# Optimization experiments

Measured on AMD Instinct MI355X. Metric: run time of the kernel, lower is better.

The kernel has to match this reference:

```python
import jax, jax.numpy as jnp
import numpy as np

TOPK = 2


def setup_inputs() -> dict:
    key = jax.random.key(0)
    k1, k2, k3, k4, k5 = jax.random.split(key, 5)
    D, H, E = 1024, 1408, 8
    hidden_states = jax.random.normal(k1, (2, 1024, D), dtype=jnp.float32)
    gate_w = jax.random.normal(k2, (E, D), dtype=jnp.float32) * 0.02
    w1g = jax.random.normal(k3, (E, D, H), dtype=jnp.float32) * 0.02
    w1u = jax.random.normal(k4, (E, D, H), dtype=jnp.float32) * 0.02
    w2 = jax.random.normal(k5, (E, H, D), dtype=jnp.float32) * 0.02
    return {"hidden_states": hidden_states, "gate_w": gate_w, "w1g": w1g, "w1u": w1u, "w2": w2}


def reference(hidden_states, gate_w, w1g, w1u, w2):
    # hidden_states: [B, S, D]; expert weights: w1g/w1u [E, D, H], w2 [E, H, D]
    B, S, D = hidden_states.shape
    E = gate_w.shape[0]
    x = hidden_states.reshape(-1, D)  # [T, D]
    T = x.shape[0]

    # --- MoEGate: softmax scores, top-k routing (no topk renorm) ---
    logits = x @ gate_w.T                      # [T, E]
    scores = jax.nn.softmax(logits, axis=-1)   # [T, E]
    topk_w, topk_idx = jax.lax.top_k(scores, TOPK)  # [T, K]

    # Per-token combine coefficient for each expert: coeff[t, e] = sum_k w[t,k] * (idx[t,k]==e)
    coeff = jnp.zeros((T, E), dtype=x.dtype).at[jnp.arange(T)[:, None], topk_idx].add(topk_w)

    # --- Grouped expert MLP (swiglu): identical math to permute + grouped GEMM + unpermute ---
    g = jnp.einsum('td,edh->teh', x, w1g)      # [T, E, H]
    u = jnp.einsum('td,edh->teh', x, w1u)      # [T, E, H]
    h = jax.nn.silu(g) * u                     # [T, E, H]
    y = jnp.einsum('teh,te,ehd->td', h, coeff, w2)  # [T, D]
    return y.reshape(B, S, D)
```

## Files before the change

kernel.cpp:

```cpp
#include <hip/hip_runtime.h>

#define TOK 2048
#define DDIM 1024
#define HDIM 1408
#define ENUM 8
#define NSLOT (2 * TOK)
#define UP_NB 22
#define UP_KS 32
#define DN_NB 16
#define DN_KS 44
#define DN_KH 22
#define TC_W1_BLK 2816
#define TC_ALL_BLK 4224
#define GATE_BLK 512

typedef unsigned int uint;
typedef unsigned short ushort;
typedef unsigned long long ull;

using bf16x8 = __attribute__((ext_vector_type(8))) __bf16;
using f32x4  = __attribute__((ext_vector_type(4))) float;

__device__ __forceinline__ float silu_f(float g) {
    return g / (1.0f + __expf(-g));
}

__device__ __forceinline__ ushort cvt_bf16(float f) {
    uint u = __float_as_uint(f);
    u += 0x7FFFu + ((u >> 16) & 1u);
    return (ushort)(u >> 16);
}

__device__ __forceinline__ void gl2lds16(const void* g, void* l) {
    __builtin_amdgcn_global_load_lds(
        (const __attribute__((address_space(1))) uint*)g,
        (__attribute__((address_space(3))) uint*)l, 16, 0, 0);
}

__global__ __launch_bounds__(256) void tcast_gate_kernel(
    const float* __restrict__ w1g, const float* __restrict__ w1u,
    const float* __restrict__ w2, ushort* __restrict__ BgP,
    ushort* __restrict__ BuP, ushort* __restrict__ W2P,
    const float* __restrict__ x, const float* __restrict__ gw,
    int* __restrict__ tinfo, float* __restrict__ wslot, ushort* __restrict__ xb)
{
    const int bid = blockIdx.x;
    const int tid = threadIdx.x;

    if (bid < TC_ALL_BLK) {
        const float* src; ushort* dst; int N, KS, NB, e, nb, ks0;
        if (bid < TC_W1_BLK) {
            const int z = bid / 176;
            const int rem = bid - z * 176;
            src = (z & 8) ? w1u : w1g;
            dst = (z & 8) ? BuP : BgP;
            N = HDIM; KS = UP_KS; NB = UP_NB; e = z & 7;
            nb = rem >> 3; ks0 = (rem & 7) * 4;
        } else {
            const int b2 = bid - TC_W1_BLK;
            e = b2 / 176;
            const int rem = b2 - e * 176;
            src = w2; dst = W2P;
            N = DDIM; KS = DN_KS; NB = DN_NB;
            nb = rem / 11; ks0 = (rem - nb * 11) * 4;
        }
        const int kg = tid & 3;
        const int nn = tid >> 2;
        const float* sb = src + (size_t)e * ((size_t)KS * 32) * N + nb * 64 + nn;
        ushort* db = dst + ((((size_t)e * NB + nb) * KS) + ks0) * 2048 + nn * 32 + kg * 8;
#pragma unroll
        for (int ksi = 0; ksi < 4; ++ksi) {
            const float* st = sb + (size_t)((ks0 + ksi) * 32 + kg * 8) * N;
            float v[8];
#pragma unroll
            for (int j = 0; j < 8; ++j) v[j] = st[(size_t)j * N];
            ushort o[8];
#pragma unroll
            for (int j = 0; j < 8; ++j) o[j] = cvt_bf16(v[j]);
            *(uint4*)(db + ksi * 2048) = *(uint4*)o;
        }
        return;
    }

    const int t = (bid - TC_ALL_BLK) * 4 + (tid >> 6);
    const int lane = tid & 63;
    const float* xr = x + (size_t)t * DDIM;
    ushort* xbr = xb + (size_t)t * DDIM;
    float xv[16];
#pragma unroll
    for (int i = 0; i < 16; ++i) xv[i] = xr[lane + 64 * i];
#pragma unroll
    for (int i = 0; i < 16; ++i) xbr[lane + 64 * i] = cvt_bf16(xv[i]);
    float logit[ENUM];
#pragma unroll
    for (int e = 0; e < ENUM; ++e) {
        const float* gr = gw + (size_t)e * DDIM;
        float acc = 0.f;
#pragma unroll
        for (int i = 0; i < 16; ++i) acc += xv[i] * gr[lane + 64 * i];
#pragma unroll
        for (int s = 32; s > 0; s >>= 1) acc += __shfl_xor(acc, s, 64);
        logit[e] = acc;
    }
    if (lane == 0) {
        float mx = logit[0];
#pragma unroll
        for (int e = 1; e < ENUM; ++e) mx = fmaxf(mx, logit[e]);
        float p[ENUM]; float se = 0.f;
#pragma unroll
        for (int e = 0; e < ENUM; ++e) { p[e] = __expf(logit[e] - mx); se += p[e]; }
        float inv = 1.0f / se;
#pragma unroll
        for (int e = 0; e < ENUM; ++e) p[e] *= inv;
        int i0 = 0;
#pragma unroll
        for (int e = 1; e < ENUM; ++e) if (p[e] > p[i0]) i0 = e;
        int i1 = (i0 == 0) ? 1 : 0;
#pragma unroll
        for (int e = 0; e < ENUM; ++e) if (e != i0 && p[e] > p[i1]) i1 = e;
        tinfo[t] = i0 | (i1 << 4);
        wslot[(t << 1)] = p[i0];
        wslot[(t << 1) | 1] = p[i1];
    }
}

__global__ __launch_bounds__(256) void gate2_kernel(
    const int* __restrict__ tinfo, int* __restrict__ counts, int* __restrict__ toks)
{
    const int e = blockIdx.x;
    const int tid = threadIdx.x;
    const int lane = tid & 63;
    __shared__ int cnt;
    if (tid == 0) cnt = 0;
    __syncthreads();
    int* te = toks + e * TOK;
    for (int t = tid; t < TOK; t += 256) {
        int info = tinfo[t];
        ull m0 = __ballot((info & 15) == e);
        if (m0) {
            int base;
            if (lane == 0) base = atomicAdd(&cnt, __popcll(m0));
            base = __shfl(base, 0, 64);
            if ((m0 >> lane) & 1)
                te[base + __popcll(m0 & ((1ull << lane) - 1))] = (t << 1);
        }
        ull m1 = __ballot((info >> 4) == e);
        if (m1) {
            int base;
            if (lane == 0) base = atomicAdd(&cnt, __popcll(m1));
            base = __shfl(base, 0, 64);
            if ((m1 >> lane) & 1)
                te[base + __popcll(m1 & ((1ull << lane) - 1))] = (t << 1) | 1;
        }
    }
    __syncthreads();
    if (tid == 0) counts[e] = cnt;
}

__global__ __launch_bounds__(256, 4) void up_mfma(
    const ushort* __restrict__ xb, const ushort* __restrict__ BgP,
    const ushort* __restrict__ BuP, const int* __restrict__ counts,
    const int* __restrict__ toks, ushort* __restrict__ Hbuf)
{
    const int e = blockIdx.z;
    const int cnt = counts[e];
    const int m0 = blockIdx.y * 128;
    if (m0 >= cnt) return;
    const int nb = blockIdx.x;
    const int tid = threadIdx.x;
    const int w = tid >> 6;
    const int lane = tid & 63;
    const int q = lane >> 4;
    const int l15 = lane & 15;
    const int wr = w >> 1;
    const int wc = w & 1;

    __shared__ ushort As[2][128][32];
    __shared__ ushort Bgs[2][64][32];
    __shared__ ushort Bus[2][64][32];
    __shared__ int rowslot[128];

    if (tid < 128) rowslot[tid] = (m0 + tid < cnt) ? toks[e * TOK + m0 + tid] : -1;
    __syncthreads();

    const int srow = w * 16 + (lane >> 2);
    const int clog = (((lane & 3) + 4 - ((srow >> 1) & 3)) & 3) * 8;
    const int as0 = rowslot[srow];
    const int as1 = rowslot[srow + 64];
    const ushort* agp0 = xb + (size_t)(as0 < 0 ? 0 : (as0 >> 1)) * DDIM + clog;
    const ushort* agp1 = xb + (size_t)(as1 < 0 ? 0 : (as1 >> 1)) * DDIM + clog;
    const size_t tb = (size_t)(e * UP_NB + nb) * UP_KS * 2048;
    const ushort* bgp = BgP + tb + srow * 32 + clog;
    const ushort* bup = BuP + tb + srow * 32 + clog;

    const int coff = ((q + (l15 >> 1)) & 3) * 8;

    f32x4 accg[4][2], accu[4][2];
#pragma unroll
    for (int i = 0; i < 4; ++i)
#pragma unroll
        for (int j = 0; j < 2; ++j) { accg[i][j] = (f32x4)0.f; accu[i][j] = (f32x4)0.f; }

#define UP_PREFETCH(KSV, B)                                        \
    {                                                              \
        gl2lds16(agp0 + (KSV) * 32, &As[B][w * 16][0]);            \
        gl2lds16(agp1 + (KSV) * 32, &As[B][64 + w * 16][0]);       \
        gl2lds16(bgp + (size_t)(KSV) * 2048, &Bgs[B][w * 16][0]);  \
        gl2lds16(bup + (size_t)(KSV) * 2048, &Bus[B][w * 16][0]);  \
    }

    UP_PREFETCH(0, 0);
    __syncthreads();

    for (int ks = 0; ks < UP_KS; ++ks) {
        const int cur = ks & 1;
        const int nxt = cur ^ 1;
        if (ks + 1 < UP_KS) UP_PREFETCH(ks + 1, nxt);

        bf16x8 a[4], bg[2], bu[2];
#pragma unroll
        for (int mi = 0; mi < 4; ++mi)
            a[mi] = *(const bf16x8*)&As[cur][wr * 64 + mi * 16 + l15][coff];
#pragma unroll
        for (int ni = 0; ni < 2; ++ni) {
            bg[ni] = *(const bf16x8*)&Bgs[cur][wc * 32 + ni * 16 + l15][coff];
            bu[ni] = *(const bf16x8*)&Bus[cur][wc * 32 + ni * 16 + l15][coff];
        }
#pragma unroll
        for (int mi = 0; mi < 4; ++mi)
#pragma unroll
            for (int ni = 0; ni < 2; ++ni) {
                accg[mi][ni] = __builtin_amdgcn_mfma_f32_16x16x32_bf16(a[mi], bg[ni], accg[mi][ni], 0, 0, 0);
                accu[mi][ni] = __builtin_amdgcn_mfma_f32_16x16x32_bf16(a[mi], bu[ni], accu[mi][ni], 0, 0, 0);
            }
        __syncthreads();
    }
#undef UP_PREFETCH

#pragma unroll
    for (int mi = 0; mi < 4; ++mi) {
#pragma unroll
        for (int r = 0; r < 4; ++r) {
            int ml = wr * 64 + mi * 16 + q * 4 + r;
            int slot = rowslot[ml];
            if (slot < 0) continue;
            ushort* hrow = Hbuf + (size_t)slot * HDIM + nb * 64 + wc * 32 + l15;
#pragma unroll
            for (int ni = 0; ni < 2; ++ni)
                hrow[ni * 16] = cvt_bf16(silu_f(accg[mi][ni][r]) * accu[mi][ni][r]);
        }
    }
}

__global__ __launch_bounds__(256, 4) void down_mfma(
    const ushort* __restrict__ Hbuf, const ushort* __restrict__ W2P,
    const int* __restrict__ counts, const int* __restrict__ toks,
    float* __restrict__ Ybuf)
{
    const int z = blockIdx.z;
    const int e = z >> 1;
    const int kh = z & 1;
    const int cnt = counts[e];
    const int m0 = blockIdx.y * 128;
    if (m0 >= cnt) return;
    const int nb = blockIdx.x;
    const int tid = threadIdx.x;
    const int w = tid >> 6;
    const int lane = tid & 63;
    const int q = lane >> 4;
    const int l15 = lane & 15;
    const int wr = w >> 1;
    const int wc = w & 1;

    __shared__ ushort As[2][128][32];
    __shared__ ushort Bs[2][128][32];
    __shared__ int rowslot[128];

    if (tid < 128) rowslot[tid] = (m0 + tid < cnt) ? toks[e * TOK + m0 + tid] : -1;
    __syncthreads();

    const int srow = w * 16 + (lane >> 2);
    const int clog = (((lane & 3) + 4 - ((srow >> 1) & 3)) & 3) * 8;
    const int as0 = rowslot[srow];
    const int as1 = rowslot[srow + 64];
    const ushort* agp0 = Hbuf + (size_t)(as0 < 0 ? 0 : as0) * HDIM + kh * (DN_KH * 32) + clog;
    const ushort* agp1 = Hbuf + (size_t)(as1 < 0 ? 0 : as1) * HDIM + kh * (DN_KH * 32) + clog;
    const int nb2 = nb * 2;
    const ushort* bp0 = W2P + ((size_t)(e * DN_NB + nb2) * DN_KS + kh * DN_KH) * 2048 + srow * 32 + clog;
    const ushort* bp1 = W2P + ((size_t)(e * DN_NB + nb2 + 1) * DN_KS + kh * DN_KH) * 2048 + srow * 32 + clog;

    const int coff = ((q + (l15 >> 1)) & 3) * 8;

    f32x4 acc[4][4];
#pragma unroll
    for (int i = 0; i < 4; ++i)
#pragma unroll
        for (int j = 0; j < 4; ++j) acc[i][j] = (f32x4)0.f;

#define DN_PREFETCH(KSV, B)                                           \
    {                                                                 \
        gl2lds16(agp0 + (KSV) * 32, &As[B][w * 16][0]);               \
        gl2lds16(agp1 + (KSV) * 32, &As[B][64 + w * 16][0]);          \
        gl2lds16(bp0 + (size_t)(KSV) * 2048, &Bs[B][w * 16][0]);      \
        gl2lds16(bp1 + (size_t)(KSV) * 2048, &Bs[B][64 + w * 16][0]); \
    }

    DN_PREFETCH(0, 0);
    __syncthreads();

    for (int ks = 0; ks < DN_KH; ++ks) {
        const int cur = ks & 1;
        const int nxt = cur ^ 1;
        if (ks + 1 < DN_KH) DN_PREFETCH(ks + 1, nxt);

        bf16x8 a[4], b[4];
#pragma unroll
        for (int mi = 0; mi < 4; ++mi)
            a[mi] = *(const bf16x8*)&As[cur][wr * 64 + mi * 16 + l15][coff];
#pragma unroll
        for (int ni = 0; ni < 4; ++ni)
            b[ni] = *(const bf16x8*)&Bs[cur][wc * 64 + ni * 16 + l15][coff];
#pragma unroll
        for (int mi = 0; mi < 4; ++mi)
#pragma unroll
            for (int ni = 0; ni < 4; ++ni)
                acc[mi][ni] = __builtin_amdgcn_mfma_f32_16x16x32_bf16(a[mi], b[ni], acc[mi][ni], 0, 0, 0);
        __syncthreads();
    }
#undef DN_PREFETCH

    float* Yp = Ybuf + (size_t)kh * NSLOT * DDIM;
#pragma unroll
    for (int mi = 0; mi < 4; ++mi) {
#pragma unroll
        for (int r = 0; r < 4; ++r) {
            int ml = wr * 64 + mi * 16 + q * 4 + r;
            int slot = rowslot[ml];
            if (slot < 0) continue;
            float* yr = Yp + (size_t)slot * DDIM + nb * 128 + wc * 64 + l15;
#pragma unroll
            for (int ni = 0; ni < 4; ++ni)
                yr[ni * 16] = acc[mi][ni][r];
        }
    }
}

__global__ __launch_bounds__(256) void combine_kernel(
    const float* __restrict__ Ybuf, const float* __restrict__ wslot,
    float* __restrict__ y)
{
    const int t = blockIdx.x;
    const int j = threadIdx.x * 4;
    const float w0 = wslot[2 * t];
    const float w1 = wslot[2 * t + 1];
    const float* y00 = Ybuf + ((size_t)2 * t) * DDIM + j;
    const float* y01 = Ybuf + ((size_t)2 * t + 1) * DDIM + j;
    const float* y10 = y00 + (size_t)NSLOT * DDIM;
    const float* y11 = y01 + (size_t)NSLOT * DDIM;
    float4 a0 = *(const float4*)y00;
    float4 b0 = *(const float4*)y01;
    float4 a1 = *(const float4*)y10;
    float4 b1 = *(const float4*)y11;
    float4 o;
    o.x = w0 * (a0.x + a1.x) + w1 * (b0.x + b1.x);
    o.y = w0 * (a0.y + a1.y) + w1 * (b0.y + b1.y);
    o.z = w0 * (a0.z + a1.z) + w1 * (b0.z + b1.z);
    o.w = w0 * (a0.w + a1.w) + w1 * (b0.w + b1.w);
    *(float4*)(y + (size_t)t * DDIM + j) = o;
}

extern "C" void kernel_launch(void* const* d_in, const int* in_sizes, int n_in,
                              void* d_out, int out_size, void* d_ws, size_t ws_size,
                              hipStream_t stream) {
    const float* x   = (const float*)d_in[0];
    const float* gw  = (const float*)d_in[1];
    const float* w1g = (const float*)d_in[2];
    const float* w1u = (const float*)d_in[3];
    const float* w2  = (const float*)d_in[4];
    float* y = (float*)d_out;
    char* ws = (char*)d_ws;

    size_t off = 0;
    int*    counts = (int*)(ws + off);   off += 256;
    int*    toks   = (int*)(ws + off);   off += (size_t)ENUM * TOK * 4;
    float*  wslot  = (float*)(ws + off); off += (size_t)NSLOT * 4;
    int*    tinfo  = (int*)(ws + off);   off += (size_t)TOK * 4;
    off = (off + 255) & ~(size_t)255;
    ushort* xb     = (ushort*)(ws + off); off += (size_t)TOK * DDIM * 2;
    size_t regA = off;
    ushort* BgP  = (ushort*)(ws + regA);
    ushort* BuP  = (ushort*)(ws + regA + (size_t)ENUM * DDIM * HDIM * 2);
    float*  Ybuf = (float*)(ws + regA);
    off = regA + (size_t)2 * ENUM * DDIM * HDIM * 2;
    ushort* W2P  = (ushort*)(ws + off);  off += (size_t)ENUM * HDIM * DDIM * 2;
    ushort* Hbuf = (ushort*)(ws + off);

    tcast_gate_kernel<<<TC_ALL_BLK + GATE_BLK, 256, 0, stream>>>(
        w1g, w1u, w2, BgP, BuP, W2P, x, gw, tinfo, wslot, xb);
    gate2_kernel<<<ENUM, 256, 0, stream>>>(tinfo, counts, toks);

    up_mfma<<<dim3(UP_NB, TOK / 128, ENUM), 256, 0, stream>>>(xb, BgP, BuP, counts, toks, Hbuf);
    down_mfma<<<dim3(DDIM / 128, TOK / 128, 16), 256, 0, stream>>>(Hbuf, W2P, counts, toks, Ybuf);
    combine_kernel<<<TOK, 256, 0, stream>>>(Ybuf, wslot, y);
}
```

Baseline: 256.2 us.

## Fuse routing scatter into gate kernel and combine via atomic adds in down GEMM

The separate gate2 routing kernel is removed. Each gate block now handles 64 tokens, builds a local histogram, reserves per-expert ranges with global atomics, and writes the token lists itself. The combine kernel and the Ybuf intermediate are also removed: down_mfma scales each row by its routing weight and atomically adds it into the zero-initialised output. This cuts two launches and a large fp32 round trip through memory. In exchange it adds two memsets, many float atomics on the output, non-deterministic summation order, and fewer gate blocks (32), each doing more serial work.

```diff
diff --git a/kernel.cpp b/kernel.cpp
--- a/kernel.cpp
+++ b/kernel.cpp
@@ -11,8 +11,8 @@
 #define DN_KS 44
 #define DN_KH 22
 #define TC_W1_BLK 2816
-#define TC_ALL_BLK 4224
-#define GATE_BLK 512
+#define CAST_ITEMS 4224
+#define GATE_BLKS 32
 
 typedef unsigned int uint;
 typedef unsigned short ushort;
@@ -42,12 +42,13 @@
     const float* __restrict__ w2, ushort* __restrict__ BgP,
     ushort* __restrict__ BuP, ushort* __restrict__ W2P,
     const float* __restrict__ x, const float* __restrict__ gw,
-    int* __restrict__ tinfo, float* __restrict__ wslot, ushort* __restrict__ xb)
+    int* __restrict__ counts, int* __restrict__ toks,
+    float* __restrict__ wslot, ushort* __restrict__ xb)
 {
     const int bid = blockIdx.x;
     const int tid = threadIdx.x;
 
-    if (bid < TC_ALL_BLK) {
+    if (bid < CAST_ITEMS) {
         const float* src; ushort* dst; int N, KS, NB, e, nb, ks0;
         if (bid < TC_W1_BLK) {
             const int z = bid / 176;
@@ -82,79 +83,71 @@
         return;
     }
 
-    const int t = (bid - TC_ALL_BLK) * 4 + (tid >> 6);
+    __shared__ int e0l[64], e1l[64];
+    __shared__ int hist[ENUM], cursor[ENUM];
+    const int base = (bid - CAST_ITEMS) * 64;
+    const int w = tid >> 6;
     const int lane = tid & 63;
-    const float* xr = x + (size_t)t * DDIM;
-    ushort* xbr = xb + (size_t)t * DDIM;
-    float xv[16];
-#pragma unroll
-    for (int i = 0; i < 16; ++i) xv[i] = xr[lane + 64 * i];
-#pragma unroll
-    for (int i = 0; i < 16; ++i) xbr[lane + 64 * i] = cvt_bf16(xv[i]);
-    float logit[ENUM];
-#pragma unroll
-    for (int e = 0; e < ENUM; ++e) {
-        const float* gr = gw + (size_t)e * DDIM;
-        float acc = 0.f;
-#pragma unroll
-        for (int i = 0; i < 16; ++i) acc += xv[i] * gr[lane + 64 * i];
-#pragma unroll
-        for (int s = 32; s > 0; s >>= 1) acc += __shfl_xor(acc, s, 64);
-        logit[e] = acc;
-    }
-    if (lane == 0) {
-        float mx = logit[0];
-#pragma unroll
-        for (int e = 1; e < ENUM; ++e) mx = fmaxf(mx, logit[e]);
-        float p[ENUM]; float se = 0.f;
-#pragma unroll
-        for (int e = 0; e < ENUM; ++e) { p[e] = __expf(logit[e] - mx); se += p[e]; }
-        float inv = 1.0f / se;
-#pragma unroll
-        for (int e = 0; e < ENUM; ++e) p[e] *= inv;
-        int i0 = 0;
-#pragma unroll
-        for (int e = 1; e < ENUM; ++e) if (p[e] > p[i0]) i0 = e;
-        int i1 = (i0 == 0) ? 1 : 0;
-#pragma unroll
-        for (int e = 0; e < ENUM; ++e) if (e != i0 && p[e] > p[i1]) i1 = e;
-        tinfo[t] = i0 | (i1 << 4);
-        wslot[(t << 1)] = p[i0];
-        wslot[(t << 1) | 1] = p[i1];
-    }
-}
-
-__global__ __launch_bounds__(256) void gate2_kernel(
-    const int* __restrict__ tinfo, int* __restrict__ counts, int* __restrict__ toks)
-{
-    const int e = blockIdx.x;
-    const int tid = threadIdx.x;
-    const int lane = tid & 63;
-    __shared__ int cnt;
-    if (tid == 0) cnt = 0;
-    __syncthreads();
-    int* te = toks + e * TOK;
-    for (int t = tid; t < TOK; t += 256) {
-        int info = tinfo[t];
-        ull m0 = __ballot((info & 15) == e);
-        if (m0) {
-            int base;
-            if (lane == 0) base = atomicAdd(&cnt, __popcll(m0));
-            base = __shfl(base, 0, 64);
-            if ((m0 >> lane) & 1)
-                te[base + __popcll(m0 & ((1ull << lane) - 1))] = (t << 1);
-        }
-        ull m1 = __ballot((info >> 4) == e);
-        if (m1) {
-            int base;
-            if (lane == 0) base = atomicAdd(&cnt, __popcll(m1));
-            base = __shfl(base, 0, 64);
-            if ((m1 >> lane) & 1)
-                te[base + __popcll(m1 & ((1ull << lane) - 1))] = (t << 1) | 1;
-        }
-    }
-    __syncthreads();
-    if (tid == 0) counts[e] = cnt;
+    if (tid < ENUM) hist[tid] = 0;
+
+    for (int it = 0; it < 16; ++it) {
+        const int lt = w * 16 + it;
+        const int t = base + lt;
+        const float* xr = x + (size_t)t * DDIM;
+        ushort* xbr = xb + (size_t)t * DDIM;
+        float xv[16];
+#pragma unroll
+        for (int i = 0; i < 16; ++i) xv[i] = xr[lane + 64 * i];
+#pragma unroll
+        for (int i = 0; i < 16; ++i) xbr[lane + 64 * i] = cvt_bf16(xv[i]);
+        float logit[ENUM];
+#pragma unroll
+        for (int e = 0; e < ENUM; ++e) {
+            const float* gr = gw + (size_t)e * DDIM;
+            float acc = 0.f;
+#pragma unroll
+            for (int i = 0; i < 16; ++i) acc += xv[i] * gr[lane + 64 * i];
+#pragma unroll
+            for (int s = 32; s > 0; s >>= 1) acc += __shfl_xor(acc, s, 64);
+            logit[e] = acc;
+        }
+        if (lane == 0) {
+            float mx = logit[0];
+#pragma unroll
+            for (int e = 1; e < ENUM; ++e) mx = fmaxf(mx, logit[e]);
+            float p[ENUM]; float se = 0.f;
+#pragma unroll
+            for (int e = 0; e < ENUM; ++e) { p[e] = __expf(logit[e] - mx); se += p[e]; }
+            float inv = 1.0f / se;
+#pragma unroll
+            for (int e = 0; e < ENUM; ++e) p[e] *= inv;
+            int i0 = 0;
+#pragma unroll
+            for (int e = 1; e < ENUM; ++e) if (p[e] > p[i0]) i0 = e;
+            int i1 = (i0 == 0) ? 1 : 0;
+#pragma unroll
+            for (int e = 0; e < ENUM; ++e) if (e != i0 && p[e] > p[i1]) i1 = e;
+            wslot[(t << 1)] = p[i0];
+            wslot[(t << 1) | 1] = p[i1];
+            e0l[lt] = i0;
+            e1l[lt] = i1;
+        }
+    }
+    __syncthreads();
+    if (tid < 64) {
+        atomicAdd(&hist[e0l[tid]], 1);
+        atomicAdd(&hist[e1l[tid]], 1);
+    }
+    __syncthreads();
+    if (tid < ENUM) cursor[tid] = atomicAdd(&counts[tid], hist[tid]);
+    __syncthreads();
+    if (tid < 64) {
+        const int t = base + tid;
+        int p0 = atomicAdd(&cursor[e0l[tid]], 1);
+        toks[e0l[tid] * TOK + p0] = (t << 1);
+        int p1 = atomicAdd(&cursor[e1l[tid]], 1);
+        toks[e1l[tid] * TOK + p1] = (t << 1) | 1;
+    }
 }
 
 __global__ __launch_bounds__(256, 4) void up_mfma(
@@ -255,7 +248,7 @@
 __global__ __launch_bounds__(256, 4) void down_mfma(
     const ushort* __restrict__ Hbuf, const ushort* __restrict__ W2P,
     const int* __restrict__ counts, const int* __restrict__ toks,
-    float* __restrict__ Ybuf)
+    const float* __restrict__ wslot, float* __restrict__ y)
 {
     const int z = blockIdx.z;
     const int e = z >> 1;
@@ -275,8 +268,13 @@
     __shared__ ushort As[2][128][32];
     __shared__ ushort Bs[2][128][32];
     __shared__ int rowslot[128];
-
-    if (tid < 128) rowslot[tid] = (m0 + tid < cnt) ? toks[e * TOK + m0 + tid] : -1;
+    __shared__ float rowwt[128];
+
+    if (tid < 128) {
+        int s = (m0 + tid < cnt) ? toks[e * TOK + m0 + tid] : -1;
+        rowslot[tid] = s;
+        rowwt[tid] = (s < 0) ? 0.f : wslot[s];
+    }
     __syncthreads();
 
     const int srow = w * 16 + (lane >> 2);
@@ -329,7 +327,6 @@
     }
 #undef DN_PREFETCH
 
-    float* Yp = Ybuf + (size_t)kh * NSLOT * DDIM;
 #pragma unroll
     for (int mi = 0; mi < 4; ++mi) {
 #pragma unroll
@@ -337,36 +334,13 @@
             int ml = wr * 64 + mi * 16 + q * 4 + r;
             int slot = rowslot[ml];
             if (slot < 0) continue;
-            float* yr = Yp + (size_t)slot * DDIM + nb * 128 + wc * 64 + l15;
+            float wv = rowwt[ml];
+            float* yr = y + (size_t)(slot >> 1) * DDIM + nb * 128 + wc * 64 + l15;
 #pragma unroll
             for (int ni = 0; ni < 4; ++ni)
-                yr[ni * 16] = acc[mi][ni][r];
-        }
-    }
-}
-
-__global__ __launch_bounds__(256) void combine_kernel(
-    const float* __restrict__ Ybuf, const float* __restrict__ wslot,
-    float* __restrict__ y)
-{
-    const int t = blockIdx.x;
-    const int j = threadIdx.x * 4;
-    const float w0 = wslot[2 * t];
-    const float w1 = wslot[2 * t + 1];
-    const float* y00 = Ybuf + ((size_t)2 * t) * DDIM + j;
-    const float* y01 = Ybuf + ((size_t)2 * t + 1) * DDIM + j;
-    const float* y10 = y00 + (size_t)NSLOT * DDIM;
-    const float* y11 = y01 + (size_t)NSLOT * DDIM;
-    float4 a0 = *(const float4*)y00;
-    float4 b0 = *(const float4*)y01;
-    float4 a1 = *(const float4*)y10;
-    float4 b1 = *(const float4*)y11;
-    float4 o;
-    o.x = w0 * (a0.x + a1.x) + w1 * (b0.x + b1.x);
-    o.y = w0 * (a0.y + a1.y) + w1 * (b0.y + b1.y);
-    o.z = w0 * (a0.z + a1.z) + w1 * (b0.z + b1.z);
-    o.w = w0 * (a0.w + a1.w) + w1 * (b0.w + b1.w);
-    *(float4*)(y + (size_t)t * DDIM + j) = o;
+                atomicAdd(&yr[ni * 16], wv * acc[mi][ni][r]);
+        }
+    }
 }
 
 extern "C" void kernel_launch(void* const* d_in, const int* in_sizes, int n_in,
@@ -384,22 +358,19 @@
     int*    counts = (int*)(ws + off);   off += 256;
     int*    toks   = (int*)(ws + off);   off += (size_t)ENUM * TOK * 4;
     float*  wslot  = (float*)(ws + off); off += (size_t)NSLOT * 4;
-    int*    tinfo  = (int*)(ws + off);   off += (size_t)TOK * 4;
     off = (off + 255) & ~(size_t)255;
     ushort* xb     = (ushort*)(ws + off); off += (size_t)TOK * DDIM * 2;
-    size_t regA = off;
-    ushort* BgP  = (ushort*)(ws + regA);
-    ushort* BuP  = (ushort*)(ws + regA + (size_t)ENUM * DDIM * HDIM * 2);
-    float*  Ybuf = (float*)(ws + regA);
-    off = regA + (size_t)2 * ENUM * DDIM * HDIM * 2;
+    ushort* BgP  = (ushort*)(ws + off);  off += (size_t)ENUM * DDIM * HDIM * 2;
+    ushort* BuP  = (ushort*)(ws + off);  off += (size_t)ENUM * DDIM * HDIM * 2;
     ushort* W2P  = (ushort*)(ws + off);  off += (size_t)ENUM * HDIM * DDIM * 2;
     ushort* Hbuf = (ushort*)(ws + off);
 
-    tcast_gate_kernel<<<TC_ALL_BLK + GATE_BLK, 256, 0, stream>>>(
-        w1g, w1u, w2, BgP, BuP, W2P, x, gw, tinfo, wslot, xb);
-    gate2_kernel<<<ENUM, 256, 0, stream>>>(tinfo, counts, toks);
+    hipMemsetAsync(counts, 0, ENUM * sizeof(int), stream);
+    hipMemsetAsync(y, 0, (size_t)TOK * DDIM * sizeof(float), stream);
+
+    tcast_gate_kernel<<<CAST_ITEMS + GATE_BLKS, 256, 0, stream>>>(
+        w1g, w1u, w2, BgP, BuP, W2P, x, gw, counts, toks, wslot, xb);
 
     up_mfma<<<dim3(UP_NB, TOK / 128, ENUM), 256, 0, stream>>>(xb, BgP, BuP, counts, toks, Hbuf);
-    down_mfma<<<dim3(DDIM / 128, TOK / 128, 16), 256, 0, stream>>>(Hbuf, W2P, counts, toks, Ybuf);
-    combine_kernel<<<TOK, 256, 0, stream>>>(Ybuf, wslot, y);
-}
+    down_mfma<<<dim3(DDIM / 128, TOK / 128, 16), 256, 0, stream>>>(Hbuf, W2P, counts, toks, wslot, y);
+}
```

After: 309.5 us. +20.8%, slower.

## Transpose-cast weights through LDS and reorder packed layout k-slab major

Applied to the files above, without the earlier changes.

The weight cast kernel now reads full 32-row K slabs with coalesced float4 loads, transposes them through a shared-memory tile, and writes bf16 in a k-slab-major packed layout. Before, each thread did strided scalar column loads. The up and down GEMM kernels change their B-pointer arithmetic to match the new layout, so consecutive k-steps now advance by a whole slab stride instead of a contiguous 2048-element tile. This targets the uncoalesced global reads in the cast stage, which handles most of the weight bytes. The cost is more blocks doing serial column loops with two barriers per iteration, and possibly worse locality for the B-tile loads in the GEMMs.

```diff
diff --git a/kernel.cpp b/kernel.cpp
--- a/kernel.cpp
+++ b/kernel.cpp
@@ -10,8 +10,8 @@
 #define DN_NB 16
 #define DN_KS 44
 #define DN_KH 22
-#define TC_W1_BLK 2816
-#define TC_ALL_BLK 4224
+#define W1C_BLK 512
+#define CAST_BLKS 864
 #define GATE_BLK 512
 
 typedef unsigned int uint;
@@ -35,6 +35,38 @@
     __builtin_amdgcn_global_load_lds(
         (const __attribute__((address_space(1))) uint*)g,
         (__attribute__((address_space(3))) uint*)l, 16, 0, 0);
+}
+
+__device__ __forceinline__ void cast_slab(
+    const float* __restrict__ src, ushort* __restrict__ dst,
+    int N, int KS, int e, int ks, int tid, float (*Ls)[132])
+{
+    const float* sb = src + (size_t)e * ((size_t)KS * 32) * N + (size_t)(ks * 32) * N;
+    ushort* db = dst + (size_t)(e * KS + ks) * N * 32;
+    const int r = tid >> 3;
+    const int c16 = (tid & 7) * 16;
+    const int nnl = tid >> 1;
+    const int kkh = (tid & 1) * 16;
+
+    for (int c0 = 0; c0 < N; c0 += 128) {
+        const float* srow = sb + (size_t)r * N + c0 + c16;
+        float4 v0 = *(const float4*)(srow + 0);
+        float4 v1 = *(const float4*)(srow + 4);
+        float4 v2 = *(const float4*)(srow + 8);
+        float4 v3 = *(const float4*)(srow + 12);
+        *(float4*)&Ls[r][c16 + 0]  = v0;
+        *(float4*)&Ls[r][c16 + 4]  = v1;
+        *(float4*)&Ls[r][c16 + 8]  = v2;
+        *(float4*)&Ls[r][c16 + 12] = v3;
+        __syncthreads();
+        ushort o[16];
+#pragma unroll
+        for (int j = 0; j < 16; ++j) o[j] = cvt_bf16(Ls[kkh + j][nnl]);
+        ushort* dt = db + (size_t)(c0 + nnl) * 32 + kkh;
+        *(uint4*)(dt + 0) = *(uint4*)(o + 0);
+        *(uint4*)(dt + 8) = *(uint4*)(o + 8);
+        __syncthreads();
+    }
 }
 
 __global__ __launch_bounds__(256) void tcast_gate_kernel(
@@ -44,45 +76,26 @@
     const float* __restrict__ x, const float* __restrict__ gw,
     int* __restrict__ tinfo, float* __restrict__ wslot, ushort* __restrict__ xb)
 {
+    __shared__ float Ls[32][132];
     const int bid = blockIdx.x;
     const int tid = threadIdx.x;
 
-    if (bid < TC_ALL_BLK) {
-        const float* src; ushort* dst; int N, KS, NB, e, nb, ks0;
-        if (bid < TC_W1_BLK) {
-            const int z = bid / 176;
-            const int rem = bid - z * 176;
-            src = (z & 8) ? w1u : w1g;
-            dst = (z & 8) ? BuP : BgP;
-            N = HDIM; KS = UP_KS; NB = UP_NB; e = z & 7;
-            nb = rem >> 3; ks0 = (rem & 7) * 4;
-        } else {
-            const int b2 = bid - TC_W1_BLK;
-            e = b2 / 176;
-            const int rem = b2 - e * 176;
-            src = w2; dst = W2P;
-            N = DDIM; KS = DN_KS; NB = DN_NB;
-            nb = rem / 11; ks0 = (rem - nb * 11) * 4;
-        }
-        const int kg = tid & 3;
-        const int nn = tid >> 2;
-        const float* sb = src + (size_t)e * ((size_t)KS * 32) * N + nb * 64 + nn;
-        ushort* db = dst + ((((size_t)e * NB + nb) * KS) + ks0) * 2048 + nn * 32 + kg * 8;
-#pragma unroll
-        for (int ksi = 0; ksi < 4; ++ksi) {
-            const float* st = sb + (size_t)((ks0 + ksi) * 32 + kg * 8) * N;
-            float v[8];
-#pragma unroll
-            for (int j = 0; j < 8; ++j) v[j] = st[(size_t)j * N];
-            ushort o[8];
-#pragma unroll
-            for (int j = 0; j < 8; ++j) o[j] = cvt_bf16(v[j]);
-            *(uint4*)(db + ksi * 2048) = *(uint4*)o;
-        }
+    if (bid < W1C_BLK) {
+        const int z = bid >> 5;
+        const int ks = bid & 31;
+        cast_slab((z & 8) ? w1u : w1g, (z & 8) ? BuP : BgP,
+                  HDIM, UP_KS, z & 7, ks, tid, Ls);
         return;
     }
-
-    const int t = (bid - TC_ALL_BLK) * 4 + (tid >> 6);
+    if (bid < CAST_BLKS) {
+        const int b2 = bid - W1C_BLK;
+        const int e = b2 / DN_KS;
+        const int ks = b2 - e * DN_KS;
+        cast_slab(w2, W2P, DDIM, DN_KS, e, ks, tid, Ls);
+        return;
+    }
+
+    const int t = (bid - CAST_BLKS) * 4 + (tid >> 6);
     const int lane = tid & 63;
     const float* xr = x + (size_t)t * DDIM;
     ushort* xbr = xb + (size_t)t * DDIM;
@@ -189,7 +202,7 @@
     const int as1 = rowslot[srow + 64];
     const ushort* agp0 = xb + (size_t)(as0 < 0 ? 0 : (as0 >> 1)) * DDIM + clog;
     const ushort* agp1 = xb + (size_t)(as1 < 0 ? 0 : (as1 >> 1)) * DDIM + clog;
-    const size_t tb = (size_t)(e * UP_NB + nb) * UP_KS * 2048;
+    const size_t tb = (size_t)e * (UP_KS * HDIM * 32) + (size_t)nb * 2048;
     const ushort* bgp = BgP + tb + srow * 32 + clog;
     const ushort* bup = BuP + tb + srow * 32 + clog;
 
@@ -201,12 +214,12 @@
 #pragma unroll
         for (int j = 0; j < 2; ++j) { accg[i][j] = (f32x4)0.f; accu[i][j] = (f32x4)0.f; }
 
-#define UP_PREFETCH(KSV, B)                                        \
-    {                                                              \
-        gl2lds16(agp0 + (KSV) * 32, &As[B][w * 16][0]);            \
-        gl2lds16(agp1 + (KSV) * 32, &As[B][64 + w * 16][0]);       \
-        gl2lds16(bgp + (size_t)(KSV) * 2048, &Bgs[B][w * 16][0]);  \
-        gl2lds16(bup + (size_t)(KSV) * 2048, &Bus[B][w * 16][0]);  \
+#define UP_PREFETCH(KSV, B)                                                    \
+    {                                                                          \
+        gl2lds16(agp0 + (KSV) * 32, &As[B][w * 16][0]);                        \
+        gl2lds16(agp1 + (KSV) * 32, &As[B][64 + w * 16][0]);                   \
+        gl2lds16(bgp + (size_t)(KSV) * (HDIM * 32), &Bgs[B][w * 16][0]);       \
+        gl2lds16(bup + (size_t)(KSV) * (HDIM * 32), &Bus[B][w * 16][0]);       \
     }
 
     UP_PREFETCH(0, 0);
@@ -285,9 +298,9 @@
     const int as1 = rowslot[srow + 64];
     const ushort* agp0 = Hbuf + (size_t)(as0 < 0 ? 0 : as0) * HDIM + kh * (DN_KH * 32) + clog;
     const ushort* agp1 = Hbuf + (size_t)(as1 < 0 ? 0 : as1) * HDIM + kh * (DN_KH * 32) + clog;
-    const int nb2 = nb * 2;
-    const ushort* bp0 = W2P + ((size_t)(e * DN_NB + nb2) * DN_KS + kh * DN_KH) * 2048 + srow * 32 + clog;
-    const ushort* bp1 = W2P + ((size_t)(e * DN_NB + nb2 + 1) * DN_KS + kh * DN_KH) * 2048 + srow * 32 + clog;
+    const size_t bb = ((size_t)e * DN_KS + kh * DN_KH) * (DDIM * 32) + (size_t)nb * 4096;
+    const ushort* bp0 = W2P + bb + srow * 32 + clog;
+    const ushort* bp1 = bp0 + 2048;
 
     const int coff = ((q + (l15 >> 1)) & 3) * 8;
 
@@ -297,12 +310,12 @@
 #pragma unroll
         for (int j = 0; j < 4; ++j) acc[i][j] = (f32x4)0.f;
 
-#define DN_PREFETCH(KSV, B)                                           \
-    {                                                                 \
-        gl2lds16(agp0 + (KSV) * 32, &As[B][w * 16][0]);               \
-        gl2lds16(agp1 + (KSV) * 32, &As[B][64 + w * 16][0]);          \
-        gl2lds16(bp0 + (size_t)(KSV) * 2048, &Bs[B][w * 16][0]);      \
-        gl2lds16(bp1 + (size_t)(KSV) * 2048, &Bs[B][64 + w * 16][0]); \
+#define DN_PREFETCH(KSV, B)                                                      \
+    {                                                                            \
+        gl2lds16(agp0 + (KSV) * 32, &As[B][w * 16][0]);                          \
+        gl2lds16(agp1 + (KSV) * 32, &As[B][64 + w * 16][0]);                     \
+        gl2lds16(bp0 + (size_t)(KSV) * (DDIM * 32), &Bs[B][w * 16][0]);          \
+        gl2lds16(bp1 + (size_t)(KSV) * (DDIM * 32), &Bs[B][64 + w * 16][0]);     \
     }
 
     DN_PREFETCH(0, 0);
@@ -395,7 +408,7 @@
     ushort* W2P  = (ushort*)(ws + off);  off += (size_t)ENUM * HDIM * DDIM * 2;
     ushort* Hbuf = (ushort*)(ws + off);
 
-    tcast_gate_kernel<<<TC_ALL_BLK + GATE_BLK, 256, 0, stream>>>(
+    tcast_gate_kernel<<<CAST_BLKS + GATE_BLK, 256, 0, stream>>>(
         w1g, w1u, w2, BgP, BuP, W2P, x, gw, tinfo, wslot, xb);
     gate2_kernel<<<ENUM, 256, 0, stream>>>(tinfo, counts, toks);
 
```

Measured after the change: 263.1 us. +2.7%, slower.

## Fuse fp32-to-bf16 weight conversion into grouped GEMM loads, drop pre-cast pass

Applied to the files above, without the earlier changes.

Removes the separate pass that cast and re-tiled all expert weights into bf16 workspace buffers. The up and down GEMM kernels now load fp32 weights directly into registers, convert them to bf16 and write them swizzled into LDS during the MFMA loop. This is meant to eliminate the full weight write/read round trip. In exchange, each M-tile block re-reads fp32 weights at twice the bytes, and the loop takes on extra register pressure and conversion work.

```diff
diff --git a/kernel.cpp b/kernel.cpp
--- a/kernel.cpp
+++ b/kernel.cpp
@@ -10,8 +10,6 @@
 #define DN_NB 16
 #define DN_KS 44
 #define DN_KH 22
-#define TC_W1_BLK 2816
-#define TC_ALL_BLK 4224
 #define GATE_BLK 512
 
 typedef unsigned int uint;
@@ -37,53 +35,12 @@
         (__attribute__((address_space(3))) uint*)l, 16, 0, 0);
 }
 
-__global__ __launch_bounds__(256) void tcast_gate_kernel(
-    const float* __restrict__ w1g, const float* __restrict__ w1u,
-    const float* __restrict__ w2, ushort* __restrict__ BgP,
-    ushort* __restrict__ BuP, ushort* __restrict__ W2P,
+__global__ __launch_bounds__(256) void gate1_kernel(
     const float* __restrict__ x, const float* __restrict__ gw,
     int* __restrict__ tinfo, float* __restrict__ wslot, ushort* __restrict__ xb)
 {
-    const int bid = blockIdx.x;
-    const int tid = threadIdx.x;
-
-    if (bid < TC_ALL_BLK) {
-        const float* src; ushort* dst; int N, KS, NB, e, nb, ks0;
-        if (bid < TC_W1_BLK) {
-            const int z = bid / 176;
-            const int rem = bid - z * 176;
-            src = (z & 8) ? w1u : w1g;
-            dst = (z & 8) ? BuP : BgP;
-            N = HDIM; KS = UP_KS; NB = UP_NB; e = z & 7;
-            nb = rem >> 3; ks0 = (rem & 7) * 4;
-        } else {
-            const int b2 = bid - TC_W1_BLK;
-            e = b2 / 176;
-            const int rem = b2 - e * 176;
-            src = w2; dst = W2P;
-            N = DDIM; KS = DN_KS; NB = DN_NB;
-            nb = rem / 11; ks0 = (rem - nb * 11) * 4;
-        }
-        const int kg = tid & 3;
-        const int nn = tid >> 2;
-        const float* sb = src + (size_t)e * ((size_t)KS * 32) * N + nb * 64 + nn;
-        ushort* db = dst + ((((size_t)e * NB + nb) * KS) + ks0) * 2048 + nn * 32 + kg * 8;
-#pragma unroll
-        for (int ksi = 0; ksi < 4; ++ksi) {
-            const float* st = sb + (size_t)((ks0 + ksi) * 32 + kg * 8) * N;
-            float v[8];
-#pragma unroll
-            for (int j = 0; j < 8; ++j) v[j] = st[(size_t)j * N];
-            ushort o[8];
-#pragma unroll
-            for (int j = 0; j < 8; ++j) o[j] = cvt_bf16(v[j]);
-            *(uint4*)(db + ksi * 2048) = *(uint4*)o;
-        }
-        return;
-    }
-
-    const int t = (bid - TC_ALL_BLK) * 4 + (tid >> 6);
-    const int lane = tid & 63;
+    const int t = blockIdx.x * 4 + (threadIdx.x >> 6);
+    const int lane = threadIdx.x & 63;
     const float* xr = x + (size_t)t * DDIM;
     ushort* xbr = xb + (size_t)t * DDIM;
     float xv[16];
@@ -158,8 +115,8 @@
 }
 
 __global__ __launch_bounds__(256, 4) void up_mfma(
-    const ushort* __restrict__ xb, const ushort* __restrict__ BgP,
-    const ushort* __restrict__ BuP, const int* __restrict__ counts,
+    const ushort* __restrict__ xb, const float* __restrict__ w1g,
+    const float* __restrict__ w1u, const int* __restrict__ counts,
     const int* __restrict__ toks, ushort* __restrict__ Hbuf)
 {
     const int e = blockIdx.z;
@@ -189,9 +146,12 @@
     const int as1 = rowslot[srow + 64];
     const ushort* agp0 = xb + (size_t)(as0 < 0 ? 0 : (as0 >> 1)) * DDIM + clog;
     const ushort* agp1 = xb + (size_t)(as1 < 0 ? 0 : (as1 >> 1)) * DDIM + clog;
-    const size_t tb = (size_t)(e * UP_NB + nb) * UP_KS * 2048;
-    const ushort* bgp = BgP + tb + srow * 32 + clog;
-    const ushort* bup = BuP + tb + srow * 32 + clog;
+
+    const int kg = lane & 3;
+    const size_t bb = (size_t)e * DDIM * HDIM + (size_t)(kg * 8) * HDIM + nb * 64 + srow;
+    const float* bg_base = w1g + bb;
+    const float* bu_base = w1u + bb;
+    const int bphys = ((kg + ((srow >> 1) & 3)) & 3) * 8;
 
     const int coff = ((q + (l15 >> 1)) & 3) * 8;
 
@@ -201,21 +161,41 @@
 #pragma unroll
         for (int j = 0; j < 2; ++j) { accg[i][j] = (f32x4)0.f; accu[i][j] = (f32x4)0.f; }
 
-#define UP_PREFETCH(KSV, B)                                        \
+    float vg[8], vu[8];
+
+#define UP_A_ISSUE(KSV, B)                              \
+    {                                                   \
+        gl2lds16(agp0 + (KSV) * 32, &As[B][w * 16][0]); \
+        gl2lds16(agp1 + (KSV) * 32, &As[B][64 + w * 16][0]); \
+    }
+#define UP_B_ISSUE(KSV)                                            \
     {                                                              \
-        gl2lds16(agp0 + (KSV) * 32, &As[B][w * 16][0]);            \
-        gl2lds16(agp1 + (KSV) * 32, &As[B][64 + w * 16][0]);       \
-        gl2lds16(bgp + (size_t)(KSV) * 2048, &Bgs[B][w * 16][0]);  \
-        gl2lds16(bup + (size_t)(KSV) * 2048, &Bus[B][w * 16][0]);  \
-    }
-
-    UP_PREFETCH(0, 0);
+        const float* bgp_ = bg_base + (size_t)(KSV) * 32 * HDIM;   \
+        const float* bup_ = bu_base + (size_t)(KSV) * 32 * HDIM;   \
+        _Pragma("unroll") for (int j = 0; j < 8; ++j) {            \
+            vg[j] = bgp_[(size_t)j * HDIM];                        \
+            vu[j] = bup_[(size_t)j * HDIM];                        \
+        }                                                          \
+    }
+#define UP_B_WRITE(B)                                              \
+    {                                                              \
+        ushort og[8], ou[8];                                       \
+        _Pragma("unroll") for (int j = 0; j < 8; ++j) {            \
+            og[j] = cvt_bf16(vg[j]); ou[j] = cvt_bf16(vu[j]);      \
+        }                                                          \
+        *(uint4*)&Bgs[B][srow][bphys] = *(uint4*)og;               \
+        *(uint4*)&Bus[B][srow][bphys] = *(uint4*)ou;               \
+    }
+
+    UP_A_ISSUE(0, 0);
+    UP_B_ISSUE(0);
+    UP_B_WRITE(0);
     __syncthreads();
 
     for (int ks = 0; ks < UP_KS; ++ks) {
         const int cur = ks & 1;
         const int nxt = cur ^ 1;
-        if (ks + 1 < UP_KS) UP_PREFETCH(ks + 1, nxt);
+        if (ks + 1 < UP_KS) { UP_A_ISSUE(ks + 1, nxt); UP_B_ISSUE(ks + 1); }
 
         bf16x8 a[4], bg[2], bu[2];
 #pragma unroll
@@ -233,9 +213,12 @@
                 accg[mi][ni] = __builtin_amdgcn_mfma_f32_16x16x32_bf16(a[mi], bg[ni], accg[mi][ni], 0, 0, 0);
                 accu[mi][ni] = __builtin_amdgcn_mfma_f32_16x16x32_bf16(a[mi], bu[ni], accu[mi][ni], 0, 0, 0);
             }
+        if (ks + 1 < UP_KS) UP_B_WRITE(nxt);
         __syncthreads();
     }
-#undef UP_PREFETCH
+#undef UP_A_ISSUE
+#undef UP_B_ISSUE
+#undef UP_B_WRITE
 
 #pragma unroll
     for (int mi = 0; mi < 4; ++mi) {
@@ -253,7 +236,7 @@
 }
 
 __global__ __launch_bounds__(256, 4) void down_mfma(
-    const ushort* __restrict__ Hbuf, const ushort* __restrict__ W2P,
+    const ushort* __restrict__ Hbuf, const float* __restrict__ w2,
     const int* __restrict__ counts, const int* __restrict__ toks,
     float* __restrict__ Ybuf)
 {
@@ -285,9 +268,11 @@
     const int as1 = rowslot[srow + 64];
     const ushort* agp0 = Hbuf + (size_t)(as0 < 0 ? 0 : as0) * HDIM + kh * (DN_KH * 32) + clog;
     const ushort* agp1 = Hbuf + (size_t)(as1 < 0 ? 0 : as1) * HDIM + kh * (DN_KH * 32) + clog;
-    const int nb2 = nb * 2;
-    const ushort* bp0 = W2P + ((size_t)(e * DN_NB + nb2) * DN_KS + kh * DN_KH) * 2048 + srow * 32 + clog;
-    const ushort* bp1 = W2P + ((size_t)(e * DN_NB + nb2 + 1) * DN_KS + kh * DN_KH) * 2048 + srow * 32 + clog;
+
+    const int kg = lane & 3;
+    const float* b_base = w2 + (size_t)e * HDIM * DDIM
+                        + (size_t)(kh * (DN_KH * 32) + kg * 8) * DDIM + nb * 128 + srow;
+    const int bphys = ((kg + ((srow >> 1) & 3)) & 3) * 8;
 
     const int coff = ((q + (l15 >> 1)) & 3) * 8;
 
@@ -297,21 +282,40 @@
 #pragma unroll
         for (int j = 0; j < 4; ++j) acc[i][j] = (f32x4)0.f;
 
-#define DN_PREFETCH(KSV, B)                                           \
-    {                                                                 \
-        gl2lds16(agp0 + (KSV) * 32, &As[B][w * 16][0]);               \
-        gl2lds16(agp1 + (KSV) * 32, &As[B][64 + w * 16][0]);          \
-        gl2lds16(bp0 + (size_t)(KSV) * 2048, &Bs[B][w * 16][0]);      \
-        gl2lds16(bp1 + (size_t)(KSV) * 2048, &Bs[B][64 + w * 16][0]); \
-    }
-
-    DN_PREFETCH(0, 0);
+    float v0[8], v1[8];
+
+#define DN_A_ISSUE(KSV, B)                              \
+    {                                                   \
+        gl2lds16(agp0 + (KSV) * 32, &As[B][w * 16][0]); \
+        gl2lds16(agp1 + (KSV) * 32, &As[B][64 + w * 16][0]); \
+    }
+#define DN_B_ISSUE(KSV)                                            \
+    {                                                              \
+        const float* bp_ = b_base + (size_t)(KSV) * 32 * DDIM;     \
+        _Pragma("unroll") for (int j = 0; j < 8; ++j) {            \
+            v0[j] = bp_[(size_t)j * DDIM];                         \
+            v1[j] = bp_[(size_t)j * DDIM + 64];                    \
+        }                                                          \
+    }
+#define DN_B_WRITE(B)                                              \
+    {                                                              \
+        ushort o0[8], o1[8];                                       \
+        _Pragma("unroll") for (int j = 0; j < 8; ++j) {            \
+            o0[j] = cvt_bf16(v0[j]); o1[j] = cvt_bf16(v1[j]);      \
+        }                                                          \
+        *(uint4*)&Bs[B][srow][bphys] = *(uint4*)o0;                \
+        *(uint4*)&Bs[B][64 + srow][bphys] = *(uint4*)o1;           \
+    }
+
+    DN_A_ISSUE(0, 0);
+    DN_B_ISSUE(0);
+    DN_B_WRITE(0);
     __syncthreads();
 
     for (int ks = 0; ks < DN_KH; ++ks) {
         const int cur = ks & 1;
         const int nxt = cur ^ 1;
-        if (ks + 1 < DN_KH) DN_PREFETCH(ks + 1, nxt);
+        if (ks + 1 < DN_KH) { DN_A_ISSUE(ks + 1, nxt); DN_B_ISSUE(ks + 1); }
 
         bf16x8 a[4], b[4];
 #pragma unroll
@@ -325,9 +329,12 @@
 #pragma unroll
             for (int ni = 0; ni < 4; ++ni)
                 acc[mi][ni] = __builtin_amdgcn_mfma_f32_16x16x32_bf16(a[mi], b[ni], acc[mi][ni], 0, 0, 0);
+        if (ks + 1 < DN_KH) DN_B_WRITE(nxt);
         __syncthreads();
     }
-#undef DN_PREFETCH
+#undef DN_A_ISSUE
+#undef DN_B_ISSUE
+#undef DN_B_WRITE
 
     float* Yp = Ybuf + (size_t)kh * NSLOT * DDIM;
 #pragma unroll
@@ -387,19 +394,13 @@
     int*    tinfo  = (int*)(ws + off);   off += (size_t)TOK * 4;
     off = (off + 255) & ~(size_t)255;
     ushort* xb     = (ushort*)(ws + off); off += (size_t)TOK * DDIM * 2;
-    size_t regA = off;
-    ushort* BgP  = (ushort*)(ws + regA);
-    ushort* BuP  = (ushort*)(ws + regA + (size_t)ENUM * DDIM * HDIM * 2);
-    float*  Ybuf = (float*)(ws + regA);
-    off = regA + (size_t)2 * ENUM * DDIM * HDIM * 2;
-    ushort* W2P  = (ushort*)(ws + off);  off += (size_t)ENUM * HDIM * DDIM * 2;
-    ushort* Hbuf = (ushort*)(ws + off);
-
-    tcast_gate_kernel<<<TC_ALL_BLK + GATE_BLK, 256, 0, stream>>>(
-        w1g, w1u, w2, BgP, BuP, W2P, x, gw, tinfo, wslot, xb);
+    ushort* Hbuf   = (ushort*)(ws + off); off += (size_t)NSLOT * HDIM * 2;
+    float*  Ybuf   = (float*)(ws + off);
+
+    gate1_kernel<<<GATE_BLK, 256, 0, stream>>>(x, gw, tinfo, wslot, xb);
     gate2_kernel<<<ENUM, 256, 0, stream>>>(tinfo, counts, toks);
 
-    up_mfma<<<dim3(UP_NB, TOK / 128, ENUM), 256, 0, stream>>>(xb, BgP, BuP, counts, toks, Hbuf);
-    down_mfma<<<dim3(DDIM / 128, TOK / 128, 16), 256, 0, stream>>>(Hbuf, W2P, counts, toks, Ybuf);
+    up_mfma<<<dim3(UP_NB, TOK / 128, ENUM), 256, 0, stream>>>(xb, w1g, w1u, counts, toks, Hbuf);
+    down_mfma<<<dim3(DDIM / 128, TOK / 128, 16), 256, 0, stream>>>(Hbuf, w2, counts, toks, Ybuf);
     combine_kernel<<<TOK, 256, 0, stream>>>(Ybuf, wslot, y);
 }
```

After: 337.4 us. +31.7%, slower.
